# Kernel tuning notes

Hardware: AMD Instinct MI355X
Metric: run time of the kernel (lower is better)

## Reference

```python
import jax, jax.numpy as jnp
import numpy as np

HEADS = 8
IN_C = 256
MDL = 512
N = 4
L = 4096
NE = 65536  # avg degree 16


def setup_inputs() -> dict:
    key = jax.random.key(0)
    ks = jax.random.split(key, 14)
    f32 = jnp.float32
    s = 0.05
    return {
        "queries": jax.random.normal(ks[0], (N, L, IN_C), f32),
        "keys": jax.random.normal(ks[1], (N, L, IN_C), f32),
        "values": jax.random.normal(ks[2], (N, L, IN_C), f32),
        "adj": jax.random.randint(ks[3], (2, NE), 0, L, dtype=jnp.int32),
        "edge_pos_enc": jax.random.normal(ks[4], (N, HEADS, NE), f32),
        "Wq": jax.random.normal(ks[5], (IN_C, MDL), f32) * s,
        "bq": jnp.zeros((MDL,), f32),
        "Wk": jax.random.normal(ks[6], (IN_C, MDL), f32) * s,
        "bk": jnp.zeros((MDL,), f32),
        "Wv": jax.random.normal(ks[7], (IN_C, MDL), f32) * s,
        "bv": jnp.zeros((MDL,), f32),
        "Wo": jax.random.normal(ks[8], (MDL, MDL), f32) * s,
        "bo": jnp.zeros((MDL,), f32),
    }


def reference(queries, keys, values, adj, edge_pos_enc, Wq, bq, Wk, bk, Wv, bv, Wo, bo):
    n, l, _ = queries.shape
    h = HEADS
    e = MDL // h  # per-head dim
    temp = 1.0 / jnp.sqrt(jnp.asarray(e, queries.dtype))
    dst, src = adj[0], adj[1]

    def split(x):  # (n, l, mdl) -> (n*h, l, e)
        return x.reshape(n, l, h, e).transpose(0, 2, 1, 3).reshape(n * h, l, e)

    q = split(queries @ Wq + bq)
    k = split(keys @ Wk + bk)
    v = split(values @ Wv + bv)
    epe = edge_pos_enc.reshape(n * h, NE)

    def head(qh, kh, vh, eh):
        # qh,kh,vh: (l, e); eh: (Ne,)
        scores = temp * (jnp.sum(qh[dst] * kh[src], axis=-1) + eh)  # (Ne,)
        m = jax.ops.segment_max(scores, dst, num_segments=l)
        p = jnp.exp(scores - m[dst])
        z = jax.ops.segment_sum(p, dst, num_segments=l)
        alpha = p / z[dst]  # segment softmax keyed by dst (adj[0])
        return jax.ops.segment_sum(alpha[:, None] * vh[src], dst, num_segments=l)  # (l, e)

    out = jax.vmap(head)(q, k, v, epe)  # (n*h, l, e)
    out = out.reshape(n, h, l, e).transpose(0, 2, 1, 3).reshape(n, l, h * e)
    return out @ Wo + bo
```

## Files before the change

### kernel.cpp

```cpp
#include <hip/hip_runtime.h>
#include <hip/hip_bf16.h>
#include <math.h>
#include <stdint.h>

#define HEADS 8
#define IN_C  256
#define MDL   512
#define NB    4
#define LL    4096
#define NE    65536
#define EDIM  64
#define TEMP  0.125f

typedef __bf16 bf16x8 __attribute__((ext_vector_type(8)));
typedef float  f32x4  __attribute__((ext_vector_type(4)));
typedef short  short8 __attribute__((ext_vector_type(8)));

__device__ __forceinline__ void glds16(const void* g, void* l) {
    __builtin_amdgcn_global_load_lds(
        (const __attribute__((address_space(1))) void*)g,
        (__attribute__((address_space(3))) void*)l, 16, 0, 0);
}

__device__ __forceinline__ short8 cvt8(float4 a, float4 b) {
    union { short8 v; __hip_bfloat16 h[8]; } u;
    u.h[0] = __float2bfloat16(a.x); u.h[1] = __float2bfloat16(a.y);
    u.h[2] = __float2bfloat16(a.z); u.h[3] = __float2bfloat16(a.w);
    u.h[4] = __float2bfloat16(b.x); u.h[5] = __float2bfloat16(b.y);
    u.h[6] = __float2bfloat16(b.z); u.h[7] = __float2bfloat16(b.w);
    return u.v;
}

__device__ __forceinline__ void tile_map(int* bm, int* bn) {
    int lin = blockIdx.y * gridDim.x + blockIdx.x;
    int xcd = lin & 7;
    int t   = lin >> 3;
    *bm = (xcd * 16 + (t & 15)) * 128;
    *bn = (t >> 4) * 128;
}

__global__ __launch_bounds__(256) void gemm_qkv(
    const float* __restrict__ A0, const float* __restrict__ A1,
    const float* __restrict__ A2,
    const __hip_bfloat16* __restrict__ B0, const __hip_bfloat16* __restrict__ B1,
    const __hip_bfloat16* __restrict__ B2,
    const float* __restrict__ b0, const float* __restrict__ b1,
    const float* __restrict__ b2,
    __hip_bfloat16* __restrict__ C0, __hip_bfloat16* __restrict__ C1,
    __hip_bfloat16* __restrict__ C2, int M, int N, int K)
{
    __shared__ __align__(16) __hip_bfloat16 As[128 * 64];
    __shared__ __align__(16) __hip_bfloat16 Bs[128 * 64];

    const int z = blockIdx.z;
    const float* A           = (z == 0) ? A0 : (z == 1) ? A1 : A2;
    const __hip_bfloat16* Bt = (z == 0) ? B0 : (z == 1) ? B1 : B2;
    const float* bias        = (z == 0) ? b0 : (z == 1) ? b1 : b2;
    __hip_bfloat16* C        = (z == 0) ? C0 : (z == 1) ? C1 : C2;

    const int tid  = threadIdx.x;
    const int lane = tid & 63;
    const int w    = tid >> 6;
    const int wr   = w >> 1, wc = w & 1;
    int bm, bn;
    tile_map(&bm, &bn);

    const float*          gA[4];
    const __hip_bfloat16* gB[4];
    __hip_bfloat16* lAw[4];
    __hip_bfloat16* lB[4];
    #pragma unroll
    for (int it = 0; it < 4; it++) {
        int idx  = it * 256 + tid;
        int r    = idx >> 3;
        int cpos = idx & 7;
        int cdat = cpos ^ (r & 7);
        gA[it]  = A  + (size_t)(bm + r) * K + cdat * 8;
        gB[it]  = Bt + (size_t)(bn + r) * K + cdat * 8;
        lAw[it] = As + r * 64 + cpos * 8;
        lB[it]  = Bs + (size_t)(it * 256 + w * 64) * 8;
    }

    int fa[2][4], fb[2][4];
    #pragma unroll
    for (int kk = 0; kk < 2; kk++)
        #pragma unroll
        for (int i = 0; i < 4; i++) {
            int rA = wr * 64 + i * 16 + (lane & 15);
            int gc = kk * 4 + (lane >> 4);
            fa[kk][i] = rA * 64 + (gc ^ (rA & 7)) * 8;
            int rB = wc * 64 + i * 16 + (lane & 15);
            fb[kk][i] = rB * 64 + (gc ^ (rB & 7)) * 8;
        }

    f32x4 acc[4][4] = {};

    for (int k0 = 0; k0 < K; k0 += 64) {
        #pragma unroll
        for (int it = 0; it < 4; it++) glds16(gB[it] + k0, lB[it]);
        #pragma unroll
        for (int it = 0; it < 4; it++) {
            float4 a = *(const float4*)(gA[it] + k0);
            float4 b = *(const float4*)(gA[it] + k0 + 4);
            *(short8*)lAw[it] = cvt8(a, b);
        }
        __syncthreads();

        #pragma unroll
        for (int kk = 0; kk < 2; kk++) {
            bf16x8 av[4], bv[4];
            #pragma unroll
            for (int i = 0; i < 4; i++) av[i] = *(const bf16x8*)(As + fa[kk][i]);
            #pragma unroll
            for (int i = 0; i < 4; i++) bv[i] = *(const bf16x8*)(Bs + fb[kk][i]);
            #pragma unroll
            for (int mi = 0; mi < 4; mi++)
                #pragma unroll
                for (int ni = 0; ni < 4; ni++)
                    acc[mi][ni] = __builtin_amdgcn_mfma_f32_16x16x32_bf16(
                        av[mi], bv[ni], acc[mi][ni], 0, 0, 0);
        }
        __syncthreads();
    }

    #pragma unroll
    for (int mi = 0; mi < 4; mi++) {
        int row = bm + wr * 64 + mi * 16 + (lane >> 4) * 4;
        #pragma unroll
        for (int ni = 0; ni < 4; ni++) {
            int col = bn + wc * 64 + ni * 16 + (lane & 15);
            float bb = bias[col];
            #pragma unroll
            for (int j = 0; j < 4; j++)
                C[(size_t)(row + j) * N + col] = __float2bfloat16(acc[mi][ni][j] + bb);
        }
    }
}

__global__ __launch_bounds__(256) void gemm_out(
    const __hip_bfloat16* __restrict__ A, const __hip_bfloat16* __restrict__ Bt,
    const float* __restrict__ bias, float* __restrict__ C, int M, int N, int K)
{
    __shared__ __align__(16) __hip_bfloat16 As[128 * 64];
    __shared__ __align__(16) __hip_bfloat16 Bs[128 * 64];

    const int tid  = threadIdx.x;
    const int lane = tid & 63;
    const int w    = tid >> 6;
    const int wr   = w >> 1, wc = w & 1;
    int bm, bn;
    tile_map(&bm, &bn);

    const __hip_bfloat16* gA[4];
    const __hip_bfloat16* gB[4];
    __hip_bfloat16* lA[4];
    __hip_bfloat16* lB[4];
    #pragma unroll
    for (int it = 0; it < 4; it++) {
        int idx = it * 256 + tid;
        int r = idx >> 3;
        int c = (idx & 7) ^ (r & 7);
        gA[it] = A  + (size_t)(bm + r) * K + c * 8;
        gB[it] = Bt + (size_t)(bn + r) * K + c * 8;
        lA[it] = As + (size_t)(it * 256 + w * 64) * 8;
        lB[it] = Bs + (size_t)(it * 256 + w * 64) * 8;
    }

    int fa[2][4], fb[2][4];
    #pragma unroll
    for (int kk = 0; kk < 2; kk++)
        #pragma unroll
        for (int i = 0; i < 4; i++) {
            int rA = wr * 64 + i * 16 + (lane & 15);
            int gc = kk * 4 + (lane >> 4);
            fa[kk][i] = rA * 64 + (gc ^ (rA & 7)) * 8;
            int rB = wc * 64 + i * 16 + (lane & 15);
            fb[kk][i] = rB * 64 + (gc ^ (rB & 7)) * 8;
        }

    f32x4 acc[4][4] = {};

    for (int k0 = 0; k0 < K; k0 += 64) {
        #pragma unroll
        for (int it = 0; it < 4; it++) {
            glds16(gA[it] + k0, lA[it]);
            glds16(gB[it] + k0, lB[it]);
        }
        __syncthreads();

        #pragma unroll
        for (int kk = 0; kk < 2; kk++) {
            bf16x8 av[4], bv[4];
            #pragma unroll
            for (int i = 0; i < 4; i++) av[i] = *(const bf16x8*)(As + fa[kk][i]);
            #pragma unroll
            for (int i = 0; i < 4; i++) bv[i] = *(const bf16x8*)(Bs + fb[kk][i]);
            #pragma unroll
            for (int mi = 0; mi < 4; mi++)
                #pragma unroll
                for (int ni = 0; ni < 4; ni++)
                    acc[mi][ni] = __builtin_amdgcn_mfma_f32_16x16x32_bf16(
                        av[mi], bv[ni], acc[mi][ni], 0, 0, 0);
        }
        __syncthreads();
    }

    #pragma unroll
    for (int mi = 0; mi < 4; mi++) {
        int row = bm + wr * 64 + mi * 16 + (lane >> 4) * 4;
        #pragma unroll
        for (int ni = 0; ni < 4; ni++) {
            int col = bn + wc * 64 + ni * 16 + (lane & 15);
            float bb = bias[col];
            #pragma unroll
            for (int j = 0; j < 4; j++)
                C[(size_t)(row + j) * N + col] = acc[mi][ni][j] + bb;
        }
    }
}

__global__ void count_edges(const int* __restrict__ dst, int* __restrict__ counts, int ne) {
    int e = blockIdx.x * blockDim.x + threadIdx.x;
    if (e < ne) atomicAdd(&counts[dst[e]], 1);
}

__global__ __launch_bounds__(1024) void scan_offsets(
    const int* __restrict__ counts, int* __restrict__ offsets,
    int* __restrict__ cursor, int* __restrict__ reorder)
{
    __shared__ int wsum[16];
    __shared__ int bcnt[9], boff[9];
    const int tid  = threadIdx.x;
    const int lane = tid & 63;
    const int wid  = tid >> 6;

    if (tid < 9) bcnt[tid] = 0;

    int c[4];
    int base = tid * 4;
    int s = 0;
    #pragma unroll
    for (int i = 0; i < 4; i++) { c[i] = counts[base + i]; s += c[i]; }

    int v = s;
    #pragma unroll
    for (int off = 1; off < 64; off <<= 1) {
        int t = __shfl_up(v, off);
        if (lane >= off) v += t;
    }
    if (lane == 63) wsum[wid] = v;
    __syncthreads();
    if (wid == 0) {
        int wv = (lane < 16) ? wsum[lane] : 0;
        #pragma unroll
        for (int off = 1; off < 16; off <<= 1) {
            int t = __shfl_up(wv, off);
            if (lane >= off) wv += t;
        }
        if (lane < 16) wsum[lane] = wv;
    }
    __syncthreads();

    int prefix = (wid > 0 ? wsum[wid - 1] : 0) + (v - s);
    int run = prefix;
    int mybk[4];
    #pragma unroll
    for (int i = 0; i < 4; i++) {
        offsets[base + i] = run;
        cursor[base + i]  = run;
        run += c[i];
        int sc = (c[i] + 7) >> 3; if (sc > 8) sc = 8;
        mybk[i] = 8 - sc;
        atomicAdd(&bcnt[mybk[i]], 1);
    }
    if (tid == 1023) offsets[4096] = run;
    __syncthreads();
    if (tid == 0) {
        int acc0 = 0;
        #pragma unroll
        for (int b = 0; b < 9; b++) { boff[b] = acc0; acc0 += bcnt[b]; }
    }
    __syncthreads();
    #pragma unroll
    for (int i = 0; i < 4; i++) {
        int pos = atomicAdd(&boff[mybk[i]], 1);
        reorder[pos] = base + i;
    }
}

__global__ __launch_bounds__(256) void prep(
    const int* __restrict__ dst, const int* __restrict__ srcarr,
    const float* __restrict__ epe, int* __restrict__ cursor,
    int* __restrict__ src_s, float* __restrict__ epe_s,
    const float* __restrict__ Wq, const float* __restrict__ Wk,
    const float* __restrict__ Wv, const float* __restrict__ Wo,
    __hip_bfloat16* __restrict__ Wqt, __hip_bfloat16* __restrict__ Wkt,
    __hip_bfloat16* __restrict__ Wvt, __hip_bfloat16* __restrict__ Wot)
{
    __shared__ float t[32][33];
    const int b = blockIdx.x;

    if (b < 256) {
        int e = b * 256 + threadIdx.x;
        int p = atomicAdd(&cursor[dst[e]], 1);
        src_s[p] = srcarr[e];
        #pragma unroll
        for (int n = 0; n < NB; n++) {
            float4 a2, b2;
            const float* base = epe + (size_t)(n * HEADS) * NE + e;
            a2.x = base[0 * NE]; a2.y = base[1 * NE]; a2.z = base[2 * NE]; a2.w = base[3 * NE];
            b2.x = base[4 * NE]; b2.y = base[5 * NE]; b2.z = base[6 * NE]; b2.w = base[7 * NE];
            float* o = epe_s + ((size_t)n * NE + p) * 8;
            *(float4*)o       = a2;
            *(float4*)(o + 4) = b2;
        }
    } else {
        int bb = b - 256;
        const float* W; __hip_bfloat16* Wt; int K, tt;
        if (bb < 384) {
            int m = bb >> 7; tt = bb & 127; K = IN_C;
            W  = (m == 0) ? Wq  : (m == 1) ? Wk  : Wv;
            Wt = (m == 0) ? Wqt : (m == 1) ? Wkt : Wvt;
        } else {
            tt = bb - 384; K = MDL; W = Wo; Wt = Wot;
        }
        const int N = MDL;
        int bx = (tt & 15) * 32;
        int by = (tt >> 4) * 32;
        int tx = threadIdx.x & 31, ty = threadIdx.x >> 5;
        #pragma unroll
        for (int i = 0; i < 4; i++)
            t[ty + i * 8][tx] = W[(size_t)(by + ty + i * 8) * N + bx + tx];
        __syncthreads();
        #pragma unroll
        for (int i = 0; i < 4; i++)
            Wt[(size_t)(bx + ty + i * 8) * K + by + tx] =
                __float2bfloat16(t[tx][ty + i * 8]);
    }
}

__global__ __launch_bounds__(256) void sparse_score(
    const __hip_bfloat16* __restrict__ Qb, const __hip_bfloat16* __restrict__ Kb,
    const int* __restrict__ src_s, const float* __restrict__ epe_s,
    const int* __restrict__ offsets, const int* __restrict__ reorder,
    float* __restrict__ score_s, float2* __restrict__ mz)
{
    const int lane = threadIdx.x & 63;
    const int wid  = threadIdx.x >> 6;
    const int bid  = blockIdx.x;
    const int xcd  = bid & 7;
    const int n    = xcd >> 1;
    const int base = ((bid >> 3) << 1) | (xcd & 1);
    const int dstn = reorder[(base << 2) | wid];
    const int task = n * LL + dstn;
    const int hg   = lane >> 3;

    const int beg = offsets[dstn];
    const int end = offsets[dstn + 1];
    const int deg = end - beg;
    if (deg == 0) return;

    bf16x8 q8 = *(const bf16x8*)(Qb + (size_t)task * MDL + lane * 8);
    float qf[8];
    #pragma unroll
    for (int j = 0; j < 8; j++) qf[j] = (float)q8[j];

    const __hip_bfloat16* Kn = Kb + (size_t)n * LL * MDL + lane * 8;
    const float* pe_n = epe_s + (size_t)n * NE * 8 + hg;
    float* sc_n = score_s + (size_t)n * NE * 8 + hg;

    float m = -INFINITY, z = 0.0f;

    if (deg <= 64) {
        const int my_src = src_s[beg + ((lane < deg) ? lane : (deg - 1))];

        #pragma unroll
        for (int slot = 0; slot < 8; slot++) {
            const int r0 = slot * 8;
            if (r0 < deg) {
                bf16x8 kk[8];
                #pragma unroll
                for (int j = 0; j < 8; j++) {
                    int s = __shfl(my_src, r0 + j);
                    kk[j] = *(const bf16x8*)(Kn + (size_t)s * MDL);
                }
                const int rel_mine = r0 + (lane & 7);
                float pp = (rel_mine < deg)
                         ? pe_n[(size_t)(beg + rel_mine) * 8] : -INFINITY;

                float p[8];
                #pragma unroll
                for (int j = 0; j < 8; j++) {
                    float d = 0.0f;
                    #pragma unroll
                    for (int dd = 0; dd < 8; dd++)
                        d = fmaf(qf[dd], (float)kk[j][dd], d);
                    p[j] = d;
                }
                float n0, n1, n2, n3, u0, u1, sraw;
                {
                    float a0 = (lane & 1) ? p[1] : p[0];
                    float b0 = (lane & 1) ? p[0] : p[1];
                    n0 = a0 + __shfl_xor(b0, 1);
                    float a1 = (lane & 1) ? p[3] : p[2];
                    float b1 = (lane & 1) ? p[2] : p[3];
                    n1 = a1 + __shfl_xor(b1, 1);
                    float a2 = (lane & 1) ? p[5] : p[4];
                    float b2 = (lane & 1) ? p[4] : p[5];
                    n2 = a2 + __shfl_xor(b2, 1);
                    float a3 = (lane & 1) ? p[7] : p[6];
                    float b3 = (lane & 1) ? p[6] : p[7];
                    n3 = a3 + __shfl_xor(b3, 1);

                    float c0 = (lane & 2) ? n1 : n0;
                    float d0 = (lane & 2) ? n0 : n1;
                    u0 = c0 + __shfl_xor(d0, 2);
                    float c1 = (lane & 2) ? n3 : n2;
                    float d1 = (lane & 2) ? n2 : n3;
                    u1 = c1 + __shfl_xor(d1, 2);

                    float e0 = (lane & 4) ? u1 : u0;
                    float f0 = (lane & 4) ? u0 : u1;
                    sraw = e0 + __shfl_xor(f0, 4);
                }

                float sc_my = TEMP * (sraw + pp);
                if (rel_mine < deg)
                    sc_n[(size_t)(beg + rel_mine) * 8] = sc_my;

                float gm = sc_my;
                gm = fmaxf(gm, __shfl_xor(gm, 1));
                gm = fmaxf(gm, __shfl_xor(gm, 2));
                gm = fmaxf(gm, __shfl_xor(gm, 4));
                float mnew = fmaxf(m, gm);
                float e_my = __expf(sc_my - mnew);
                float gs = e_my;
                gs += __shfl_xor(gs, 1);
                gs += __shfl_xor(gs, 2);
                gs += __shfl_xor(gs, 4);
                z = z * __expf(m - mnew) + gs;
                m = mnew;
            }
        }
    } else {
        for (int i = beg; i < end; i += 4) {
            float sc4[4];
            #pragma unroll
            for (int j = 0; j < 4; j++) {
                int idx = i + j;
                int ok  = idx < end;
                int s   = ok ? src_s[idx] : src_s[beg];
                bf16x8 kk = *(const bf16x8*)(Kn + (size_t)s * MDL);
                float pp = ok ? pe_n[(size_t)idx * 8] : -INFINITY;
                float d = 0.0f;
                #pragma unroll
                for (int dd = 0; dd < 8; dd++) d += qf[dd] * (float)kk[dd];
                d += __shfl_xor(d, 1);
                d += __shfl_xor(d, 2);
                d += __shfl_xor(d, 4);
                sc4[j] = TEMP * (d + pp);
                if (ok && (lane & 7) == 0)
                    sc_n[(size_t)idx * 8] = sc4[j];
            }
            float mb   = fmaxf(fmaxf(sc4[0], sc4[1]), fmaxf(sc4[2], sc4[3]));
            float mnew = fmaxf(m, mb);
            float sc   = __expf(m - mnew);
            float s0 = __expf(sc4[0] - mnew);
            float s1 = __expf(sc4[1] - mnew);
            float s2 = __expf(sc4[2] - mnew);
            float s3 = __expf(sc4[3] - mnew);
            z = z * sc + (s0 + s1 + s2 + s3);
            m = mnew;
        }
    }

    if ((lane & 7) == 0) {
        float2 v; v.x = m; v.y = 1.0f / z;
        mz[(size_t)task * 8 + hg] = v;
    }
}

__global__ __launch_bounds__(256) void sparse_out(
    const __hip_bfloat16* __restrict__ Vb,
    const int* __restrict__ src_s, const float* __restrict__ score_s,
    const int* __restrict__ offsets, const int* __restrict__ reorder,
    const float2* __restrict__ mz, __hip_bfloat16* __restrict__ O)
{
    const int lane = threadIdx.x & 63;
    const int wid  = threadIdx.x >> 6;
    const int bid  = blockIdx.x;
    const int xcd  = bid & 7;
    const int n    = xcd >> 1;
    const int base = ((bid >> 3) << 1) | (xcd & 1);
    const int dstn = reorder[(base << 2) | wid];
    const int task = n * LL + dstn;
    const int hg   = lane >> 3;

    const size_t rowbase = (size_t)task * MDL;
    const int beg = offsets[dstn];
    const int end = offsets[dstn + 1];
    const int deg = end - beg;

    union { short8 v8; __hip_bfloat16 h[8]; } uo;
    if (deg == 0) {
        #pragma unroll
        for (int j = 0; j < 8; j++) uo.h[j] = __float2bfloat16(0.0f);
        *(short8*)(O + rowbase + lane * 8) = uo.v8;
        return;
    }

    float2 mzv = mz[(size_t)task * 8 + hg];
    const float m = mzv.x, zinv = mzv.y;

    const __hip_bfloat16* Vn = Vb + (size_t)n * LL * MDL + lane * 8;
    const float* sc_n = score_s + (size_t)n * NE * 8 + hg;

    float acc[8] = {};

    if (deg <= 64) {
        const int my_src = src_s[beg + ((lane < deg) ? lane : (deg - 1))];

        #pragma unroll
        for (int slot = 0; slot < 8; slot++) {
            const int r0 = slot * 8;
            if (r0 < deg) {
                bf16x8 vv[8];
                #pragma unroll
                for (int j = 0; j < 8; j++) {
                    int s = __shfl(my_src, r0 + j);
                    vv[j] = *(const bf16x8*)(Vn + (size_t)s * MDL);
                }
                const int rel_mine = r0 + (lane & 7);
                float sc = (rel_mine < deg)
                         ? sc_n[(size_t)(beg + rel_mine) * 8] : -INFINITY;
                float a_l = __expf(sc - m) * zinv;
                #pragma unroll
                for (int j = 0; j < 8; j++) {
                    float al = __shfl(a_l, (lane & 56) | j);
                    #pragma unroll
                    for (int dd = 0; dd < 8; dd++)
                        acc[dd] = fmaf(al, (float)vv[j][dd], acc[dd]);
                }
            }
        }
    } else {
        for (int i = beg; i < end; i += 4) {
            #pragma unroll
            for (int j = 0; j < 4; j++) {
                int idx = i + j;
                int ok  = idx < end;
                int s   = ok ? src_s[idx] : src_s[beg];
                bf16x8 vv = *(const bf16x8*)(Vn + (size_t)s * MDL);
                float sc = ok ? sc_n[(size_t)idx * 8] : -INFINITY;
                float al = __expf(sc - m) * zinv;
                #pragma unroll
                for (int dd = 0; dd < 8; dd++)
                    acc[dd] = fmaf(al, (float)vv[dd], acc[dd]);
            }
        }
    }

    #pragma unroll
    for (int j = 0; j < 8; j++) uo.h[j] = __float2bfloat16(acc[j]);
    *(short8*)(O + rowbase + lane * 8) = uo.v8;
}

extern "C" void kernel_launch(void* const* d_in, const int* in_sizes, int n_in,
                              void* d_out, int out_size, void* d_ws, size_t ws_size,
                              hipStream_t stream)
{
    const float* queries = (const float*)d_in[0];
    const float* keys    = (const float*)d_in[1];
    const float* values  = (const float*)d_in[2];
    const int*   adj     = (const int*)d_in[3];
    const float* epe     = (const float*)d_in[4];
    const float* Wq = (const float*)d_in[5];
    const float* bq = (const float*)d_in[6];
    const float* Wk = (const float*)d_in[7];
    const float* bk = (const float*)d_in[8];
    const float* Wv = (const float*)d_in[9];
    const float* bv = (const float*)d_in[10];
    const float* Wo = (const float*)d_in[11];
    const float* bo = (const float*)d_in[12];
    float* out = (float*)d_out;

    const int* dst = adj;
    const int* src = adj + NE;

    const int    M   = NB * LL;
    const size_t NLM = (size_t)M * MDL;

    char* w = (char*)d_ws;
    __hip_bfloat16* Qb  = (__hip_bfloat16*)w; w += NLM * 2;
    __hip_bfloat16* Kb  = (__hip_bfloat16*)w; w += NLM * 2;
    __hip_bfloat16* Vb  = (__hip_bfloat16*)w; w += NLM * 2;
    __hip_bfloat16* Ob  = (__hip_bfloat16*)w; w += NLM * 2;
    __hip_bfloat16* Wqt = (__hip_bfloat16*)w; w += (size_t)MDL * IN_C * 2;
    __hip_bfloat16* Wkt = (__hip_bfloat16*)w; w += (size_t)MDL * IN_C * 2;
    __hip_bfloat16* Wvt = (__hip_bfloat16*)w; w += (size_t)MDL * IN_C * 2;
    __hip_bfloat16* Wot = (__hip_bfloat16*)w; w += (size_t)MDL * MDL * 2;
    int* counts  = (int*)w; w += 4096 * sizeof(int);
    int* offsets = (int*)w; w += 4100 * sizeof(int);
    int* cursor  = (int*)w; w += 4096 * sizeof(int);
    int* reorder = (int*)w; w += 4096 * sizeof(int);
    int*   src_s = (int*)w; w += NE * sizeof(int);
    float* epe_s   = (float*)w;  w += (size_t)NB * NE * 8 * sizeof(float);
    float* score_s = (float*)w;  w += (size_t)NB * NE * 8 * sizeof(float);
    float2* mz     = (float2*)w; w += (size_t)M * 8 * sizeof(float2);

    hipMemsetAsync(counts, 0, 4096 * sizeof(int), stream);
    count_edges<<<NE / 256, 256, 0, stream>>>(dst, counts, NE);
    scan_offsets<<<1, 1024, 0, stream>>>(counts, offsets, cursor, reorder);

    prep<<<896, 256, 0, stream>>>(dst, src, epe, cursor, src_s, epe_s,
                                  Wq, Wk, Wv, Wo, Wqt, Wkt, Wvt, Wot);

    dim3 g3(MDL / 128, M / 128, 3);
    gemm_qkv<<<g3, 256, 0, stream>>>(queries, keys, values, Wqt, Wkt, Wvt,
                                     bq, bk, bv, Qb, Kb, Vb, M, MDL, IN_C);

    sparse_score<<<(NB * LL) / 4, 256, 0, stream>>>(Qb, Kb, src_s, epe_s,
                                                    offsets, reorder, score_s, mz);
    sparse_out<<<(NB * LL) / 4, 256, 0, stream>>>(Vb, src_s, score_s,
                                                  offsets, reorder, mz, Ob);

    dim3 g(MDL / 128, M / 128);
    gemm_out<<<g, 256, 0, stream>>>(Ob, Wot, bo, out, M, MDL, MDL);
}
```

Before: 123.2 us.

## Double-buffer GEMM LDS tiles and fuse CSR histogram into single-block build kernel

Both GEMM kernels now use two LDS buffers and prefetch the next K tile (global-to-LDS loads for B, register-staged fp32 loads for A in the QKV GEMM) while the MFMAs run on the current tile. Each K step then needs one barrier instead of two, and load latency overlaps compute. Separately, the memset, global-atomic count kernel and scan kernel are merged into one 1024-thread kernel that builds the degree histogram with LDS atomics. This removes two launches and a memset, but the histogram now runs on a single block, and the doubled LDS use may lower GEMM occupancy.

```diff
diff --git a/kernel.cpp b/kernel.cpp
--- a/kernel.cpp
+++ b/kernel.cpp
@@ -49,8 +49,8 @@
     __hip_bfloat16* __restrict__ C0, __hip_bfloat16* __restrict__ C1,
     __hip_bfloat16* __restrict__ C2, int M, int N, int K)
 {
-    __shared__ __align__(16) __hip_bfloat16 As[128 * 64];
-    __shared__ __align__(16) __hip_bfloat16 Bs[128 * 64];
+    __shared__ __align__(16) __hip_bfloat16 As[2][128 * 64];
+    __shared__ __align__(16) __hip_bfloat16 Bs[2][128 * 64];
 
     const int z = blockIdx.z;
     const float* A           = (z == 0) ? A0 : (z == 1) ? A1 : A2;
@@ -67,8 +67,7 @@
 
     const float*          gA[4];
     const __hip_bfloat16* gB[4];
-    __hip_bfloat16* lAw[4];
-    __hip_bfloat16* lB[4];
+    int lAoff[4], lBoff[4];
     #pragma unroll
     for (int it = 0; it < 4; it++) {
         int idx  = it * 256 + tid;
@@ -77,8 +76,8 @@
         int cdat = cpos ^ (r & 7);
         gA[it]  = A  + (size_t)(bm + r) * K + cdat * 8;
         gB[it]  = Bt + (size_t)(bn + r) * K + cdat * 8;
-        lAw[it] = As + r * 64 + cpos * 8;
-        lB[it]  = Bs + (size_t)(it * 256 + w * 64) * 8;
+        lAoff[it] = r * 64 + cpos * 8;
+        lBoff[it] = (it * 256 + w * 64) * 8;
     }
 
     int fa[2][4], fb[2][4];
@@ -95,24 +94,44 @@
 
     f32x4 acc[4][4] = {};
 
+    #pragma unroll
+    for (int it = 0; it < 4; it++) glds16(gB[it], &Bs[0][lBoff[it]]);
+    {
+        float4 p0[4], p1[4];
+        #pragma unroll
+        for (int it = 0; it < 4; it++) {
+            p0[it] = *(const float4*)(gA[it]);
+            p1[it] = *(const float4*)(gA[it] + 4);
+        }
+        #pragma unroll
+        for (int it = 0; it < 4; it++)
+            *(short8*)&As[0][lAoff[it]] = cvt8(p0[it], p1[it]);
+    }
+    __syncthreads();
+
+    int cur = 0;
     for (int k0 = 0; k0 < K; k0 += 64) {
-        #pragma unroll
-        for (int it = 0; it < 4; it++) glds16(gB[it] + k0, lB[it]);
-        #pragma unroll
-        for (int it = 0; it < 4; it++) {
-            float4 a = *(const float4*)(gA[it] + k0);
-            float4 b = *(const float4*)(gA[it] + k0 + 4);
-            *(short8*)lAw[it] = cvt8(a, b);
-        }
-        __syncthreads();
+        const int nxt = cur ^ 1;
+        const bool has_next = (k0 + 64 < K);
+        float4 p0[4], p1[4];
+        if (has_next) {
+            #pragma unroll
+            for (int it = 0; it < 4; it++)
+                glds16(gB[it] + k0 + 64, &Bs[nxt][lBoff[it]]);
+            #pragma unroll
+            for (int it = 0; it < 4; it++) {
+                p0[it] = *(const float4*)(gA[it] + k0 + 64);
+                p1[it] = *(const float4*)(gA[it] + k0 + 64 + 4);
+            }
+        }
 
         #pragma unroll
         for (int kk = 0; kk < 2; kk++) {
             bf16x8 av[4], bv[4];
             #pragma unroll
-            for (int i = 0; i < 4; i++) av[i] = *(const bf16x8*)(As + fa[kk][i]);
-            #pragma unroll
-            for (int i = 0; i < 4; i++) bv[i] = *(const bf16x8*)(Bs + fb[kk][i]);
+            for (int i = 0; i < 4; i++) av[i] = *(const bf16x8*)&As[cur][fa[kk][i]];
+            #pragma unroll
+            for (int i = 0; i < 4; i++) bv[i] = *(const bf16x8*)&Bs[cur][fb[kk][i]];
             #pragma unroll
             for (int mi = 0; mi < 4; mi++)
                 #pragma unroll
@@ -120,7 +139,14 @@
                     acc[mi][ni] = __builtin_amdgcn_mfma_f32_16x16x32_bf16(
                         av[mi], bv[ni], acc[mi][ni], 0, 0, 0);
         }
+
+        if (has_next) {
+            #pragma unroll
+            for (int it = 0; it < 4; it++)
+                *(short8*)&As[nxt][lAoff[it]] = cvt8(p0[it], p1[it]);
+        }
         __syncthreads();
+        cur = nxt;
     }
 
     #pragma unroll
@@ -141,8 +167,8 @@
     const __hip_bfloat16* __restrict__ A, const __hip_bfloat16* __restrict__ Bt,
     const float* __restrict__ bias, float* __restrict__ C, int M, int N, int K)
 {
-    __shared__ __align__(16) __hip_bfloat16 As[128 * 64];
-    __shared__ __align__(16) __hip_bfloat16 Bs[128 * 64];
+    __shared__ __align__(16) __hip_bfloat16 As[2][128 * 64];
+    __shared__ __align__(16) __hip_bfloat16 Bs[2][128 * 64];
 
     const int tid  = threadIdx.x;
     const int lane = tid & 63;
@@ -153,8 +179,7 @@
 
     const __hip_bfloat16* gA[4];
     const __hip_bfloat16* gB[4];
-    __hip_bfloat16* lA[4];
-    __hip_bfloat16* lB[4];
+    int lAoff[4], lBoff[4];
     #pragma unroll
     for (int it = 0; it < 4; it++) {
         int idx = it * 256 + tid;
@@ -162,8 +187,8 @@
         int c = (idx & 7) ^ (r & 7);
         gA[it] = A  + (size_t)(bm + r) * K + c * 8;
         gB[it] = Bt + (size_t)(bn + r) * K + c * 8;
-        lA[it] = As + (size_t)(it * 256 + w * 64) * 8;
-        lB[it] = Bs + (size_t)(it * 256 + w * 64) * 8;
+        lAoff[it] = (it * 256 + w * 64) * 8;
+        lBoff[it] = (it * 256 + w * 64) * 8;
     }
 
     int fa[2][4], fb[2][4];
@@ -180,21 +205,31 @@
 
     f32x4 acc[4][4] = {};
 
+    #pragma unroll
+    for (int it = 0; it < 4; it++) {
+        glds16(gA[it], &As[0][lAoff[it]]);
+        glds16(gB[it], &Bs[0][lBoff[it]]);
+    }
+    __syncthreads();
+
+    int cur = 0;
     for (int k0 = 0; k0 < K; k0 += 64) {
-        #pragma unroll
-        for (int it = 0; it < 4; it++) {
-            glds16(gA[it] + k0, lA[it]);
-            glds16(gB[it] + k0, lB[it]);
-        }
-        __syncthreads();
+        const int nxt = cur ^ 1;
+        if (k0 + 64 < K) {
+            #pragma unroll
+            for (int it = 0; it < 4; it++) {
+                glds16(gA[it] + k0 + 64, &As[nxt][lAoff[it]]);
+                glds16(gB[it] + k0 + 64, &Bs[nxt][lBoff[it]]);
+            }
+        }
 
         #pragma unroll
         for (int kk = 0; kk < 2; kk++) {
             bf16x8 av[4], bv[4];
             #pragma unroll
-            for (int i = 0; i < 4; i++) av[i] = *(const bf16x8*)(As + fa[kk][i]);
-            #pragma unroll
-            for (int i = 0; i < 4; i++) bv[i] = *(const bf16x8*)(Bs + fb[kk][i]);
+            for (int i = 0; i < 4; i++) av[i] = *(const bf16x8*)&As[cur][fa[kk][i]];
+            #pragma unroll
+            for (int i = 0; i < 4; i++) bv[i] = *(const bf16x8*)&Bs[cur][fb[kk][i]];
             #pragma unroll
             for (int mi = 0; mi < 4; mi++)
                 #pragma unroll
@@ -203,6 +238,7 @@
                         av[mi], bv[ni], acc[mi][ni], 0, 0, 0);
         }
         __syncthreads();
+        cur = nxt;
     }
 
     #pragma unroll
@@ -219,28 +255,38 @@
     }
 }
 
-__global__ void count_edges(const int* __restrict__ dst, int* __restrict__ counts, int ne) {
-    int e = blockIdx.x * blockDim.x + threadIdx.x;
-    if (e < ne) atomicAdd(&counts[dst[e]], 1);
-}
-
-__global__ __launch_bounds__(1024) void scan_offsets(
-    const int* __restrict__ counts, int* __restrict__ offsets,
+__global__ __launch_bounds__(1024) void csr_build(
+    const int* __restrict__ dst, int* __restrict__ offsets,
     int* __restrict__ cursor, int* __restrict__ reorder)
 {
+    __shared__ int hist[4096];
     __shared__ int wsum[16];
     __shared__ int bcnt[9], boff[9];
     const int tid  = threadIdx.x;
     const int lane = tid & 63;
     const int wid  = tid >> 6;
 
+    #pragma unroll
+    for (int i = 0; i < 4; i++) hist[tid + i * 1024] = 0;
     if (tid < 9) bcnt[tid] = 0;
+    __syncthreads();
+
+    const int4* d4 = (const int4*)dst;
+    #pragma unroll
+    for (int i = 0; i < 16; i++) {
+        int4 v = d4[i * 1024 + tid];
+        atomicAdd(&hist[v.x], 1);
+        atomicAdd(&hist[v.y], 1);
+        atomicAdd(&hist[v.z], 1);
+        atomicAdd(&hist[v.w], 1);
+    }
+    __syncthreads();
 
     int c[4];
     int base = tid * 4;
     int s = 0;
     #pragma unroll
-    for (int i = 0; i < 4; i++) { c[i] = counts[base + i]; s += c[i]; }
+    for (int i = 0; i < 4; i++) { c[i] = hist[base + i]; s += c[i]; }
 
     int v = s;
     #pragma unroll
@@ -599,7 +645,6 @@
     __hip_bfloat16* Wkt = (__hip_bfloat16*)w; w += (size_t)MDL * IN_C * 2;
     __hip_bfloat16* Wvt = (__hip_bfloat16*)w; w += (size_t)MDL * IN_C * 2;
     __hip_bfloat16* Wot = (__hip_bfloat16*)w; w += (size_t)MDL * MDL * 2;
-    int* counts  = (int*)w; w += 4096 * sizeof(int);
     int* offsets = (int*)w; w += 4100 * sizeof(int);
     int* cursor  = (int*)w; w += 4096 * sizeof(int);
     int* reorder = (int*)w; w += 4096 * sizeof(int);
@@ -608,9 +653,7 @@
     float* score_s = (float*)w;  w += (size_t)NB * NE * 8 * sizeof(float);
     float2* mz     = (float2*)w; w += (size_t)M * 8 * sizeof(float2);
 
-    hipMemsetAsync(counts, 0, 4096 * sizeof(int), stream);
-    count_edges<<<NE / 256, 256, 0, stream>>>(dst, counts, NE);
-    scan_offsets<<<1, 1024, 0, stream>>>(counts, offsets, cursor, reorder);
+    csr_build<<<1, 1024, 0, stream>>>(dst, offsets, cursor, reorder);
 
     prep<<<896, 256, 0, stream>>>(dst, src, epe, cursor, src_s, epe_s,
                                   Wq, Wk, Wv, Wo, Wqt, Wkt, Wvt, Wot);
```

Measured after the change: 123.0 us. No clear change (-0.2%).
